# Optimization experiments

Measured on AMD Instinct MI355X. Metric: run time of the kernel, lower is better.

Reference implementation:

```python
import jax, jax.numpy as jnp
import numpy as np

EMBD = 256
HEAD = 4
HD = EMBD // HEAD  # 64
EPS = 1e-5


def setup_inputs() -> dict:
    key = jax.random.key(0)
    ks = jax.random.split(key, 12)
    s = lambda fan_in: 1.0 / np.sqrt(fan_in)
    return {
        "x": jax.random.normal(ks[0], (16, 1024, EMBD), dtype=jnp.float32),
        # attention params (stored as [in, out])
        "qkv_w": jax.random.uniform(ks[1], (EMBD, 3 * EMBD), jnp.float32, -s(EMBD), s(EMBD)),
        "qkv_b": jax.random.uniform(ks[2], (3 * EMBD,), jnp.float32, -s(EMBD), s(EMBD)),
        "out_w": jax.random.uniform(ks[3], (EMBD, EMBD), jnp.float32, -s(EMBD), s(EMBD)),
        "out_b": jax.random.uniform(ks[4], (EMBD,), jnp.float32, -s(EMBD), s(EMBD)),
        # MLP params
        "fc_w": jax.random.uniform(ks[5], (EMBD, 4 * EMBD), jnp.float32, -s(EMBD), s(EMBD)),
        "fc_b": jax.random.uniform(ks[6], (4 * EMBD,), jnp.float32, -s(EMBD), s(EMBD)),
        "proj_w": jax.random.uniform(ks[7], (4 * EMBD, EMBD), jnp.float32, -s(4 * EMBD), s(4 * EMBD)),
        "proj_b": jax.random.uniform(ks[8], (EMBD,), jnp.float32, -s(4 * EMBD), s(4 * EMBD)),
        # LayerNorm params
        "ln1_g": jnp.ones((EMBD,), jnp.float32),
        "ln1_b": jnp.zeros((EMBD,), jnp.float32),
        "ln2_g": jnp.ones((EMBD,), jnp.float32),
        "ln2_b": jnp.zeros((EMBD,), jnp.float32),
    }


def layer_norm(x, g, b):
    mu = jnp.mean(x, axis=-1, keepdims=True)
    var = jnp.mean(jnp.square(x - mu), axis=-1, keepdims=True)
    return (x - mu) * jax.lax.rsqrt(var + EPS) * g + b


def block_forward(x, qkv_w, qkv_b, out_w, out_b, fc_w, fc_b, proj_w, proj_b,
                  ln1_g, ln1_b, ln2_g, ln2_b):
    B, S, E = x.shape
    # --- attention branch ---
    h = layer_norm(x, ln1_g, ln1_b)
    qkv = h @ qkv_w + qkv_b                       # [B,S,3E]
    q, k, v = jnp.split(qkv, 3, axis=-1)
    q = q.reshape(B, S, HEAD, HD).transpose(0, 2, 1, 3)  # [B,H,S,D]
    k = k.reshape(B, S, HEAD, HD).transpose(0, 2, 1, 3)
    v = v.reshape(B, S, HEAD, HD).transpose(0, 2, 1, 3)
    att = jnp.einsum('bhqd,bhkd->bhqk', q, k) / jnp.sqrt(jnp.float32(HD))
    causal = jnp.tril(jnp.ones((S, S), dtype=bool))
    att = jnp.where(causal, att, -jnp.inf)
    att = jax.nn.softmax(att, axis=-1)
    o = jnp.einsum('bhqk,bhkd->bhqd', att, v)     # [B,H,S,D]
    o = o.transpose(0, 2, 1, 3).reshape(B, S, E)
    x = x + o @ out_w + out_b
    # --- MLP branch (dropout inactive at eval) ---
    h = layer_norm(x, ln2_g, ln2_b)
    h = jax.nn.relu(h @ fc_w + fc_b)
    x = x + h @ proj_w + proj_b
    return x


def reference(x, qkv_w, qkv_b, out_w, out_b, fc_w, fc_b, proj_w, proj_b,
              ln1_g, ln1_b, ln2_g, ln2_b):
    return block_forward(x, qkv_w, qkv_b, out_w, out_b, fc_w, fc_b,
                         proj_w, proj_b, ln1_g, ln1_b, ln2_g, ln2_b)
```

## Files before the change

### kernel.cpp

```cpp
#include <hip/hip_runtime.h>
#include <cstdint>


using f32x4 = __attribute__((ext_vector_type(4))) float;
using s16x8 = __attribute__((ext_vector_type(8))) short;
using s16x4 = __attribute__((ext_vector_type(4))) short;

__device__ inline short f2bf(float f) {
    union { float f; unsigned u; } v{f};
    unsigned r = (v.u + 0x7FFFu + ((v.u >> 16) & 1u)) >> 16;
    return (short)r;
}

__device__ inline void gload16(const void* g, void* l) {
    __builtin_amdgcn_global_load_lds(
        (const __attribute__((address_space(1))) void*)g,
        (__attribute__((address_space(3))) void*)l, 16, 0, 0);
}

__global__ __launch_bounds__(256) void wconv_all_kernel(
    const float* __restrict__ qkv_w, const float* __restrict__ out_w,
    const float* __restrict__ fc_w,  const float* __restrict__ proj_w,
    short* __restrict__ wt_qkv, short* __restrict__ wt_out,
    short* __restrict__ wt_fc,  short* __restrict__ wt_proj)
{
    __shared__ short T[64][65];
    int id = blockIdx.x;
    const float* W; short* Wt; int K, N, nt, kt;
    if (id < 48)       { W = qkv_w;  Wt = wt_qkv;  K = 256;  N = 768;  nt = id % 12;        kt = id / 12; }
    else if (id < 64)  { W = out_w;  Wt = wt_out;  K = 256;  N = 256;  nt = (id - 48) & 3;  kt = (id - 48) >> 2; }
    else if (id < 128) { W = fc_w;   Wt = wt_fc;   K = 256;  N = 1024; nt = (id - 64) & 15; kt = (id - 64) >> 4; }
    else               { W = proj_w; Wt = wt_proj; K = 1024; N = 256;  nt = (id - 128) & 3; kt = (id - 128) >> 2; }
    int n0 = nt * 64, k0 = kt * 64;

    int tid = threadIdx.x;
    int r  = tid >> 2;
    int c  = (tid & 3) << 4;

    const float* src = W + (size_t)(k0 + r) * N + n0 + c;
#pragma unroll
    for (int u = 0; u < 4; ++u) {
        float4 v = *reinterpret_cast<const float4*>(src + u * 4);
        T[r][c + u * 4 + 0] = f2bf(v.x);
        T[r][c + u * 4 + 1] = f2bf(v.y);
        T[r][c + u * 4 + 2] = f2bf(v.z);
        T[r][c + u * 4 + 3] = f2bf(v.w);
    }
    __syncthreads();
    s16x8 o0, o1;
#pragma unroll
    for (int j = 0; j < 8; ++j) { o0[j] = T[c + j][r]; o1[j] = T[c + 8 + j][r]; }
    short* dst = Wt + (size_t)(n0 + r) * K + k0 + c;
    *reinterpret_cast<s16x8*>(dst)     = o0;
    *reinterpret_cast<s16x8*>(dst + 8) = o1;
}

__global__ __launch_bounds__(256) void ln_kernel(const float* __restrict__ x,
                                                 const float* __restrict__ gamma,
                                                 const float* __restrict__ beta,
                                                 short* __restrict__ out)
{
    int tid  = threadIdx.x;
    int lane = tid & 63;
    int row  = blockIdx.x * 4 + (tid >> 6);
    const float* xr = x + (size_t)row * 256;
    float4 v = *reinterpret_cast<const float4*>(xr + lane * 4);

    float s = v.x + v.y + v.z + v.w;
#pragma unroll
    for (int o = 32; o >= 1; o >>= 1) s += __shfl_xor(s, o);
    float mu = s * (1.0f / 256.0f);

    float dx = v.x - mu, dy = v.y - mu, dz = v.z - mu, dw = v.w - mu;
    float q = dx * dx + dy * dy + dz * dz + dw * dw;
#pragma unroll
    for (int o = 32; o >= 1; o >>= 1) q += __shfl_xor(q, o);
    float rstd = rsqrtf(q * (1.0f / 256.0f) + 1e-5f);

    float4 gv = *reinterpret_cast<const float4*>(gamma + lane * 4);
    float4 bv = *reinterpret_cast<const float4*>(beta + lane * 4);
    s16x4 ov;
    ov[0] = f2bf(dx * rstd * gv.x + bv.x);
    ov[1] = f2bf(dy * rstd * gv.y + bv.y);
    ov[2] = f2bf(dz * rstd * gv.z + bv.z);
    ov[3] = f2bf(dw * rstd * gv.w + bv.w);
    *reinterpret_cast<s16x4*>(out + (size_t)row * 256 + lane * 4) = ov;
}

template <int RELU, int RES, int OBF16, int BM>
__global__ __launch_bounds__(256) void mgemm_kernel(const short* __restrict__ A,
                                                    const short* __restrict__ Bt,
                                                    const float* __restrict__ bias,
                                                    const float* __restrict__ R,
                                                    void* __restrict__ Cv,
                                                    int N, int K)
{
    constexpr int MI = BM / 32;
    __shared__ short As[BM * 64];
    __shared__ short Bs[128 * 64];

    int tid = threadIdx.x;
    int l   = tid & 63;
    int w   = tid >> 6;
    int lr  = l & 15;
    int lk8 = (l >> 4) << 3;
    int r4  = (l >> 4) << 2;
    int wr  = w >> 1, wc = w & 1;
    int bn  = blockIdx.x * 128, bm = blockIdx.y * BM;

    int scolS = ((l & 7) << 3) ^ ((l >> 3) << 3);
    int srowA = w * (BM / 4) + (l >> 3);
    int srowB = (w << 5) + (l >> 3);
    const short* pa = A  + (size_t)(bm + srowA) * K + scolS;
    const short* pb = Bt + (size_t)(bn + srowB) * K + scolS;
    short* dstA = As + w * (BM / 4) * 64;
    short* dstB = Bs + (w << 11);

    f32x4 acc[MI][4];
#pragma unroll
    for (int mi = 0; mi < MI; ++mi)
#pragma unroll
        for (int ni = 0; ni < 4; ++ni) acc[mi][ni] = (f32x4){0.f, 0.f, 0.f, 0.f};

    int swz = (lr & 7) << 3;

    for (int k0 = 0; k0 < K; k0 += 64) {
        __syncthreads();
#pragma unroll
        for (int i = 0; i < BM / 32; ++i)
            gload16(pa + (size_t)(i * 8) * K + k0, dstA + (i << 9));
#pragma unroll
        for (int i = 0; i < 4; ++i)
            gload16(pb + (size_t)(i * 8) * K + k0, dstB + (i << 9));
        __syncthreads();

#pragma unroll
        for (int ks = 0; ks < 2; ++ks) {
            s16x8 af[MI], bf[4];
#pragma unroll
            for (int mi = 0; mi < MI; ++mi) {
                int row = wr * (BM / 2) + (mi << 4) + lr;
                af[mi] = *reinterpret_cast<const s16x8*>(
                    &As[(row << 6) + (((ks << 5) + lk8) ^ swz)]);
            }
#pragma unroll
            for (int ni = 0; ni < 4; ++ni) {
                int row = (wc << 6) + (ni << 4) + lr;
                bf[ni] = *reinterpret_cast<const s16x8*>(
                    &Bs[(row << 6) + (((ks << 5) + lk8) ^ swz)]);
            }
#pragma unroll
            for (int mi = 0; mi < MI; ++mi)
#pragma unroll
                for (int ni = 0; ni < 4; ++ni)
                    acc[mi][ni] = __builtin_amdgcn_mfma_f32_16x16x32_bf16(
                        af[mi], bf[ni], acc[mi][ni], 0, 0, 0);
        }
    }

    float bv[4];
#pragma unroll
    for (int ni = 0; ni < 4; ++ni)
        bv[ni] = bias[bn + (wc << 6) + (ni << 4) + lr];

#pragma unroll
    for (int mi = 0; mi < MI; ++mi) {
#pragma unroll
        for (int ni = 0; ni < 4; ++ni) {
            int n = bn + (wc << 6) + (ni << 4) + lr;
#pragma unroll
            for (int r = 0; r < 4; ++r) {
                int m = bm + wr * (BM / 2) + (mi << 4) + r4 + r;
                float v = acc[mi][ni][r] + bv[ni];
                if (RELU) v = fmaxf(v, 0.0f);
                if (RES)  v += R[(size_t)m * N + n];
                if (OBF16) ((short*)Cv)[(size_t)m * N + n] = f2bf(v);
                else       ((float*)Cv)[(size_t)m * N + n] = v;
            }
        }
    }
}

__global__ __launch_bounds__(256) void oproj_ln_kernel(const short* __restrict__ A,
                                                       const short* __restrict__ Bt,
                                                       const float* __restrict__ bias,
                                                       const float* __restrict__ R,
                                                       float* __restrict__ x1,
                                                       short* __restrict__ h2,
                                                       const float* __restrict__ g,
                                                       const float* __restrict__ bb)
{
    __shared__ short As[64 * 64];
    __shared__ short Bs[256 * 64];

    int tid = threadIdx.x;
    int l   = tid & 63;
    int w   = tid >> 6;
    int lr  = l & 15;
    int lk8 = (l >> 4) << 3;
    int r4  = (l >> 4) << 2;
    int bm  = blockIdx.x * 64;

    int scolS = ((l & 7) << 3) ^ ((l >> 3) << 3);
    const short* pa = A  + (size_t)(bm + (w << 4) + (l >> 3)) * 256 + scolS;
    const short* pb = Bt + (size_t)((w << 6) + (l >> 3)) * 256 + scolS;
    short* dstA = As + (w << 10);
    short* dstB = Bs + (w << 12);

    f32x4 acc[16];
#pragma unroll
    for (int ni = 0; ni < 16; ++ni) acc[ni] = (f32x4){0.f, 0.f, 0.f, 0.f};

    int swz = (lr & 7) << 3;

    for (int k0 = 0; k0 < 256; k0 += 64) {
        __syncthreads();
#pragma unroll
        for (int i = 0; i < 2; ++i)
            gload16(pa + (size_t)(i * 8) * 256 + k0, dstA + (i << 9));
#pragma unroll
        for (int i = 0; i < 8; ++i)
            gload16(pb + (size_t)(i * 8) * 256 + k0, dstB + (i << 9));
        __syncthreads();

#pragma unroll
        for (int ks = 0; ks < 2; ++ks) {
            int arow = (w << 4) + lr;
            s16x8 af = *reinterpret_cast<const s16x8*>(
                &As[(arow << 6) + (((ks << 5) + lk8) ^ swz)]);
#pragma unroll
            for (int ni = 0; ni < 16; ++ni) {
                int row = (ni << 4) + lr;
                s16x8 bf = *reinterpret_cast<const s16x8*>(
                    &Bs[(row << 6) + (((ks << 5) + lk8) ^ swz)]);
                acc[ni] = __builtin_amdgcn_mfma_f32_16x16x32_bf16(af, bf, acc[ni], 0, 0, 0);
            }
        }
    }

#pragma unroll
    for (int ni = 0; ni < 16; ++ni) {
        int n = (ni << 4) + lr;
        float bvx = bias[n];
#pragma unroll
        for (int r = 0; r < 4; ++r) {
            int m = bm + (w << 4) + r4 + r;
            acc[ni][r] += bvx + R[(size_t)m * 256 + n];
        }
    }
#pragma unroll
    for (int r = 0; r < 4; ++r) {
        float s = 0.0f;
#pragma unroll
        for (int ni = 0; ni < 16; ++ni) s += acc[ni][r];
        s += __shfl_xor(s, 1); s += __shfl_xor(s, 2);
        s += __shfl_xor(s, 4); s += __shfl_xor(s, 8);
        float mu = s * (1.0f / 256.0f);
        float q = 0.0f;
#pragma unroll
        for (int ni = 0; ni < 16; ++ni) {
            float d = acc[ni][r] - mu;
            q += d * d;
        }
        q += __shfl_xor(q, 1); q += __shfl_xor(q, 2);
        q += __shfl_xor(q, 4); q += __shfl_xor(q, 8);
        float rstd = rsqrtf(q * (1.0f / 256.0f) + 1e-5f);

        int m = bm + (w << 4) + r4 + r;
#pragma unroll
        for (int ni = 0; ni < 16; ++ni) {
            int n = (ni << 4) + lr;
            float v = acc[ni][r];
            x1[(size_t)m * 256 + n] = v;
            h2[(size_t)m * 256 + n] = f2bf((v - mu) * rstd * g[n] + bb[n]);
        }
    }
}

__global__ __launch_bounds__(256) void attn_kernel(const short* __restrict__ qkv,
                                                   short* __restrict__ o)
{
    __shared__ short Ks[128 * 64];
    __shared__ short Vt[2 * 64 * 64];
    __shared__ short QP[64 * 128];

    int bid  = blockIdx.x;
    int slot = bid & 7;
    int kk2  = bid >> 3;
    int pair = kk2 & 7;
    int bh   = slot + ((kk2 >> 3) << 3);
    int b = bh >> 2, h = bh & 3;

    int tid  = threadIdx.x;
    const short* base = qkv + (size_t)b * 1024 * 768;

    int l   = tid & 63;
    int w   = tid >> 6;
    int lr  = l & 15;
    int lk8 = (l >> 4) << 3;
    int r4  = (l >> 4) << 2;
    int w16 = w << 4;

    const float SC = 0.125f * 1.44269504088896f;

    for (int sel = 0; sel < 2; ++sel) {
        int qt = sel == 0 ? pair : 15 - pair;

        __syncthreads();
        {
            int qr = tid >> 2;
            int c0 = (tid & 3) << 4;
            int sw = (qr & 7) << 3;
            const short* qg = base + (size_t)(qt * 64 + qr) * 768 + h * 64 + c0;
            s16x8 q0 = *reinterpret_cast<const s16x8*>(qg);
            s16x8 q1 = *reinterpret_cast<const s16x8*>(qg + 8);
            *reinterpret_cast<s16x8*>(&QP[qr * 128 + (c0 ^ sw)])       = q0;
            *reinterpret_cast<s16x8*>(&QP[qr * 128 + ((c0 + 8) ^ sw)]) = q1;
        }
        __syncthreads();

        s16x8 qf[2];
#pragma unroll
        for (int ks = 0; ks < 2; ++ks) {
            int row = w16 + lr;
            qf[ks] = *reinterpret_cast<const s16x8*>(
                &QP[row * 128 + ((lk8 + 32 * ks) ^ ((row & 7) << 3))]);
        }

        float m[4], lsum[4];
        f32x4 oacc[4];
#pragma unroll
        for (int r = 0; r < 4; ++r) { m[r] = -1e30f; lsum[r] = 0.0f; }
#pragma unroll
        for (int jt = 0; jt < 4; ++jt) oacc[jt] = (f32x4){0.f, 0.f, 0.f, 0.f};

        int ntile = qt >> 1;
        for (int kt = 0; kt <= ntile; ++kt) {
            __syncthreads();
            {
                int c0 = (tid & 3) << 4;
#pragma unroll
                for (int i = 0; i < 2; ++i) {
                    int krow = i * 64 + (tid >> 2);
                    const short* kg = base + (size_t)(kt * 128 + krow) * 768 + 256 + h * 64 + c0;
                    s16x8 k0v = *reinterpret_cast<const s16x8*>(kg);
                    s16x8 k1v = *reinterpret_cast<const s16x8*>(kg + 8);
                    int sw = (krow & 7) << 3;
                    *reinterpret_cast<s16x8*>(&Ks[krow * 64 + (c0 ^ sw)])       = k0v;
                    *reinterpret_cast<s16x8*>(&Ks[krow * 64 + ((c0 + 8) ^ sw)]) = k1v;
                    s16x8 v0 = *reinterpret_cast<const s16x8*>(kg + 256);
                    s16x8 v1 = *reinterpret_cast<const s16x8*>(kg + 264);
                    short* vth = Vt + ((krow >> 6) << 12);
                    int kkl = krow & 63;
#pragma unroll
                    for (int e = 0; e < 8; ++e) {
                        int da = c0 + e, db = c0 + 8 + e;
                        vth[da * 64 + (kkl ^ ((da & 7) << 3))] = v0[e];
                        vth[db * 64 + (kkl ^ ((db & 7) << 3))] = v1[e];
                    }
                }
            }
            __syncthreads();

            f32x4 s[8];
#pragma unroll
            for (int jt = 0; jt < 8; ++jt) s[jt] = (f32x4){0.f, 0.f, 0.f, 0.f};
#pragma unroll
            for (int ks = 0; ks < 2; ++ks) {
#pragma unroll
                for (int jt = 0; jt < 8; ++jt) {
                    int row = jt * 16 + lr;
                    s16x8 kf = *reinterpret_cast<const s16x8*>(
                        &Ks[row * 64 + ((lk8 + 32 * ks) ^ ((lr & 7) << 3))]);
                    s[jt] = __builtin_amdgcn_mfma_f32_16x16x32_bf16(qf[ks], kf, s[jt], 0, 0, 0);
                }
            }
#pragma unroll
            for (int jt = 0; jt < 8; ++jt)
#pragma unroll
                for (int r = 0; r < 4; ++r) s[jt][r] *= SC;

            if (kt == ntile) {
#pragma unroll
                for (int jt = 0; jt < 8; ++jt)
#pragma unroll
                    for (int r = 0; r < 4; ++r)
                        if (kt * 128 + jt * 16 + lr > qt * 64 + w16 + r4 + r)
                            s[jt][r] = -1e30f;
            }

#pragma unroll
            for (int r = 0; r < 4; ++r) {
                float rm = s[0][r];
#pragma unroll
                for (int jt = 1; jt < 8; ++jt) rm = fmaxf(rm, s[jt][r]);
                rm = fmaxf(rm, __shfl_xor(rm, 1));
                rm = fmaxf(rm, __shfl_xor(rm, 2));
                rm = fmaxf(rm, __shfl_xor(rm, 4));
                rm = fmaxf(rm, __shfl_xor(rm, 8));
                float mn  = fmaxf(m[r], rm);
                float fct = exp2f(m[r] - mn);
                m[r] = mn;
                float p[8], ps = 0.0f;
#pragma unroll
                for (int jt = 0; jt < 8; ++jt) { p[jt] = exp2f(s[jt][r] - mn); ps += p[jt]; }
                ps += __shfl_xor(ps, 1);
                ps += __shfl_xor(ps, 2);
                ps += __shfl_xor(ps, 4);
                ps += __shfl_xor(ps, 8);
                lsum[r] = lsum[r] * fct + ps;
#pragma unroll
                for (int jt = 0; jt < 4; ++jt) oacc[jt][r] *= fct;
                int row = w16 + r4 + r;
                int sw  = (row & 15) << 3;
                int rb  = row * 128;
#pragma unroll
                for (int jt = 0; jt < 8; ++jt)
                    QP[rb + ((lr + 16 * jt) ^ sw)] = f2bf(p[jt]);
            }

            int prow = w16 + lr;
            int psw  = (prow & 15) << 3;
#pragma unroll
            for (int ks = 0; ks < 4; ++ks) {
                s16x8 pf = *reinterpret_cast<const s16x8*>(
                    &QP[prow * 128 + ((lk8 + 32 * ks) ^ psw)]);
                const short* vth = Vt + ((ks >> 1) << 12);
#pragma unroll
                for (int jt = 0; jt < 4; ++jt) {
                    int vrow = jt * 16 + lr;
                    s16x8 vf = *reinterpret_cast<const s16x8*>(
                        &vth[vrow * 64 + ((((ks & 1) << 5) + lk8) ^ ((lr & 7) << 3))]);
                    oacc[jt] = __builtin_amdgcn_mfma_f32_16x16x32_bf16(pf, vf, oacc[jt], 0, 0, 0);
                }
            }
        }

#pragma unroll
        for (int r = 0; r < 4; ++r) {
            float inv = 1.0f / lsum[r];
            short* orow = o + (size_t)(b * 1024 + qt * 64 + w16 + r4 + r) * 256 + h * 64;
#pragma unroll
            for (int jt = 0; jt < 4; ++jt)
                orow[lr + 16 * jt] = f2bf(oacc[jt][r] * inv);
        }
    }
}

extern "C" void kernel_launch(void* const* d_in, const int* in_sizes, int n_in,
                              void* d_out, int out_size, void* d_ws, size_t ws_size,
                              hipStream_t stream)
{
    const float* x      = (const float*)d_in[0];
    const float* qkv_w  = (const float*)d_in[1];
    const float* qkv_b  = (const float*)d_in[2];
    const float* out_w  = (const float*)d_in[3];
    const float* out_b  = (const float*)d_in[4];
    const float* fc_w   = (const float*)d_in[5];
    const float* fc_b   = (const float*)d_in[6];
    const float* proj_w = (const float*)d_in[7];
    const float* proj_b = (const float*)d_in[8];
    const float* ln1_g  = (const float*)d_in[9];
    const float* ln1_b  = (const float*)d_in[10];
    const float* ln2_g  = (const float*)d_in[11];
    const float* ln2_b  = (const float*)d_in[12];
    float* out = (float*)d_out;

    short* ws = (short*)d_ws;
    short* wt_qkv  = ws;
    short* wt_out  = ws + 196608;
    short* wt_fc   = ws + 262144;
    short* wt_proj = ws + 524288;
    short* bufA    = ws + 786432;
    short* bufB    = ws + 4980736;

    dim3 blk(256);

    wconv_all_kernel<<<dim3(192), blk, 0, stream>>>(
        qkv_w, out_w, fc_w, proj_w, wt_qkv, wt_out, wt_fc, wt_proj);
    ln_kernel<<<dim3(4096), blk, 0, stream>>>(x, ln1_g, ln1_b, bufA);
    mgemm_kernel<0, 0, 1, 128><<<dim3(6, 128), blk, 0, stream>>>(
        bufA, wt_qkv, qkv_b, nullptr, bufB, 768, 256);
    attn_kernel<<<dim3(512), blk, 0, stream>>>(bufB, bufA);
    oproj_ln_kernel<<<dim3(256), blk, 0, stream>>>(
        bufA, wt_out, out_b, x, out, bufA, ln2_g, ln2_b);
    mgemm_kernel<1, 0, 1, 128><<<dim3(8, 128), blk, 0, stream>>>(
        bufA, wt_fc, fc_b, nullptr, bufB, 1024, 256);
    mgemm_kernel<0, 1, 0, 64><<<dim3(2, 256), blk, 0, stream>>>(
        bufB, wt_proj, proj_b, out, out, 256, 1024);
}
```

Before: 138.5 us.

## Keep softmax probabilities in registers via permlane swaps and split attention grid

The attention kernel now computes S transposed (K as the A operand), so each lane holds a column of scores for one query row. It then packs probabilities to bf16 with v_cvt_pk_bf16_f32 and rearranges them with permlane32/16 swaps into the PV MFMA operand layout, removing the LDS round-trip through the QP buffer. The paired query-tile loop per block is replaced by one query tile per block, which doubles the grid to 1024 blocks, and launch bounds request 4 blocks per CU. This adds more blocks with uneven causal work and relies on the cross-lane shuffle layout being correct.

```diff
diff --git a/kernel.cpp b/kernel.cpp
--- a/kernel.cpp
+++ b/kernel.cpp
@@ -10,6 +10,18 @@
     union { float f; unsigned u; } v{f};
     unsigned r = (v.u + 0x7FFFu + ((v.u >> 16) & 1u)) >> 16;
     return (short)r;
+}
+
+__device__ inline int cvt_pk_bf16(float lo, float hi) {
+    int d;
+    asm("v_cvt_pk_bf16_f32 %0, %1, %2" : "=v"(d) : "v"(lo), "v"(hi));
+    return d;
+}
+__device__ inline void swap32(int& a, int& b) {
+    asm("v_permlane32_swap_b32 %0, %1" : "+v"(a), "+v"(b));
+}
+__device__ inline void swap16(int& a, int& b) {
+    asm("v_permlane16_swap_b32 %0, %1" : "+v"(a), "+v"(b));
 }
 
 __device__ inline void gload16(const void* g, void* l) {
@@ -277,173 +289,180 @@
     }
 }
 
-__global__ __launch_bounds__(256) void attn_kernel(const short* __restrict__ qkv,
-                                                   short* __restrict__ o)
+__global__ __launch_bounds__(256, 4) void attn_kernel(const short* __restrict__ qkv,
+                                                      short* __restrict__ o)
 {
+    __shared__ short Qs[64 * 64];
     __shared__ short Ks[128 * 64];
     __shared__ short Vt[2 * 64 * 64];
-    __shared__ short QP[64 * 128];
 
     int bid  = blockIdx.x;
-    int slot = bid & 7;
-    int kk2  = bid >> 3;
-    int pair = kk2 & 7;
-    int bh   = slot + ((kk2 >> 3) << 3);
+    int xcd  = bid & 7;
+    int rest = bid >> 3;
+    int qt   = rest & 15;
+    int bh   = ((rest >> 4) << 3) | xcd;
     int b = bh >> 2, h = bh & 3;
 
-    int tid  = threadIdx.x;
+    int tid = threadIdx.x;
     const short* base = qkv + (size_t)b * 1024 * 768;
 
     int l   = tid & 63;
     int w   = tid >> 6;
     int lr  = l & 15;
-    int lk8 = (l >> 4) << 3;
-    int r4  = (l >> 4) << 2;
+    int g   = l >> 4;
+    int lk8 = g << 3;
     int w16 = w << 4;
+    int qglob = qt * 64 + w16 + lr;
 
     const float SC = 0.125f * 1.44269504088896f;
 
-    for (int sel = 0; sel < 2; ++sel) {
-        int qt = sel == 0 ? pair : 15 - pair;
-
+    {
+        int qr = tid >> 2;
+        int c0 = (tid & 3) << 4;
+        int sw = (qr & 7) << 3;
+        const short* qg = base + (size_t)(qt * 64 + qr) * 768 + h * 64 + c0;
+        s16x8 q0 = *reinterpret_cast<const s16x8*>(qg);
+        s16x8 q1 = *reinterpret_cast<const s16x8*>(qg + 8);
+        *reinterpret_cast<s16x8*>(&Qs[qr * 64 + (c0 ^ sw)])       = q0;
+        *reinterpret_cast<s16x8*>(&Qs[qr * 64 + ((c0 + 8) ^ sw)]) = q1;
+    }
+    __syncthreads();
+
+    s16x8 qf[2];
+#pragma unroll
+    for (int ks = 0; ks < 2; ++ks) {
+        int row = w16 + lr;
+        qf[ks] = *reinterpret_cast<const s16x8*>(
+            &Qs[row * 64 + ((32 * ks + lk8) ^ ((lr & 7) << 3))]);
+    }
+
+    float m = -1e30f, lsum = 0.0f;
+    f32x4 oacc[4];
+#pragma unroll
+    for (int dt = 0; dt < 4; ++dt) oacc[dt] = (f32x4){0.f, 0.f, 0.f, 0.f};
+
+    int ntile = qt >> 1;
+    for (int kt = 0; kt <= ntile; ++kt) {
         __syncthreads();
         {
-            int qr = tid >> 2;
             int c0 = (tid & 3) << 4;
-            int sw = (qr & 7) << 3;
-            const short* qg = base + (size_t)(qt * 64 + qr) * 768 + h * 64 + c0;
-            s16x8 q0 = *reinterpret_cast<const s16x8*>(qg);
-            s16x8 q1 = *reinterpret_cast<const s16x8*>(qg + 8);
-            *reinterpret_cast<s16x8*>(&QP[qr * 128 + (c0 ^ sw)])       = q0;
-            *reinterpret_cast<s16x8*>(&QP[qr * 128 + ((c0 + 8) ^ sw)]) = q1;
+#pragma unroll
+            for (int i = 0; i < 2; ++i) {
+                int krow = i * 64 + (tid >> 2);
+                const short* kg = base + (size_t)(kt * 128 + krow) * 768 + 256 + h * 64 + c0;
+                s16x8 k0v = *reinterpret_cast<const s16x8*>(kg);
+                s16x8 k1v = *reinterpret_cast<const s16x8*>(kg + 8);
+                int sw = (krow & 7) << 3;
+                *reinterpret_cast<s16x8*>(&Ks[krow * 64 + (c0 ^ sw)])       = k0v;
+                *reinterpret_cast<s16x8*>(&Ks[krow * 64 + ((c0 + 8) ^ sw)]) = k1v;
+                s16x8 v0 = *reinterpret_cast<const s16x8*>(kg + 256);
+                s16x8 v1 = *reinterpret_cast<const s16x8*>(kg + 264);
+                short* vth = Vt + ((krow >> 6) << 12);
+                int kkl = krow & 63;
+#pragma unroll
+                for (int e = 0; e < 8; ++e) {
+                    int da = c0 + e, db = c0 + 8 + e;
+                    vth[da * 64 + (kkl ^ ((da & 7) << 3))] = v0[e];
+                    vth[db * 64 + (kkl ^ ((db & 7) << 3))] = v1[e];
+                }
+            }
         }
         __syncthreads();
 
-        s16x8 qf[2];
+        f32x4 s[8];
+#pragma unroll
+        for (int jt = 0; jt < 8; ++jt) s[jt] = (f32x4){0.f, 0.f, 0.f, 0.f};
 #pragma unroll
         for (int ks = 0; ks < 2; ++ks) {
-            int row = w16 + lr;
-            qf[ks] = *reinterpret_cast<const s16x8*>(
-                &QP[row * 128 + ((lk8 + 32 * ks) ^ ((row & 7) << 3))]);
-        }
-
-        float m[4], lsum[4];
-        f32x4 oacc[4];
-#pragma unroll
-        for (int r = 0; r < 4; ++r) { m[r] = -1e30f; lsum[r] = 0.0f; }
-#pragma unroll
-        for (int jt = 0; jt < 4; ++jt) oacc[jt] = (f32x4){0.f, 0.f, 0.f, 0.f};
-
-        int ntile = qt >> 1;
-        for (int kt = 0; kt <= ntile; ++kt) {
-            __syncthreads();
-            {
-                int c0 = (tid & 3) << 4;
-#pragma unroll
-                for (int i = 0; i < 2; ++i) {
-                    int krow = i * 64 + (tid >> 2);
-                    const short* kg = base + (size_t)(kt * 128 + krow) * 768 + 256 + h * 64 + c0;
-                    s16x8 k0v = *reinterpret_cast<const s16x8*>(kg);
-                    s16x8 k1v = *reinterpret_cast<const s16x8*>(kg + 8);
-                    int sw = (krow & 7) << 3;
-                    *reinterpret_cast<s16x8*>(&Ks[krow * 64 + (c0 ^ sw)])       = k0v;
-                    *reinterpret_cast<s16x8*>(&Ks[krow * 64 + ((c0 + 8) ^ sw)]) = k1v;
-                    s16x8 v0 = *reinterpret_cast<const s16x8*>(kg + 256);
-                    s16x8 v1 = *reinterpret_cast<const s16x8*>(kg + 264);
-                    short* vth = Vt + ((krow >> 6) << 12);
-                    int kkl = krow & 63;
-#pragma unroll
-                    for (int e = 0; e < 8; ++e) {
-                        int da = c0 + e, db = c0 + 8 + e;
-                        vth[da * 64 + (kkl ^ ((da & 7) << 3))] = v0[e];
-                        vth[db * 64 + (kkl ^ ((db & 7) << 3))] = v1[e];
-                    }
-                }
-            }
-            __syncthreads();
-
-            f32x4 s[8];
-#pragma unroll
-            for (int jt = 0; jt < 8; ++jt) s[jt] = (f32x4){0.f, 0.f, 0.f, 0.f};
-#pragma unroll
-            for (int ks = 0; ks < 2; ++ks) {
-#pragma unroll
-                for (int jt = 0; jt < 8; ++jt) {
-                    int row = jt * 16 + lr;
-                    s16x8 kf = *reinterpret_cast<const s16x8*>(
-                        &Ks[row * 64 + ((lk8 + 32 * ks) ^ ((lr & 7) << 3))]);
-                    s[jt] = __builtin_amdgcn_mfma_f32_16x16x32_bf16(qf[ks], kf, s[jt], 0, 0, 0);
-                }
-            }
-#pragma unroll
-            for (int jt = 0; jt < 8; ++jt)
-#pragma unroll
-                for (int r = 0; r < 4; ++r) s[jt][r] *= SC;
-
-            if (kt == ntile) {
-#pragma unroll
-                for (int jt = 0; jt < 8; ++jt)
-#pragma unroll
-                    for (int r = 0; r < 4; ++r)
-                        if (kt * 128 + jt * 16 + lr > qt * 64 + w16 + r4 + r)
-                            s[jt][r] = -1e30f;
-            }
-
+#pragma unroll
+            for (int jt = 0; jt < 8; ++jt) {
+                int row = jt * 16 + lr;
+                s16x8 kf = *reinterpret_cast<const s16x8*>(
+                    &Ks[row * 64 + ((32 * ks + lk8) ^ ((lr & 7) << 3))]);
+                s[jt] = __builtin_amdgcn_mfma_f32_16x16x32_bf16(kf, qf[ks], s[jt], 0, 0, 0);
+            }
+        }
+#pragma unroll
+        for (int jt = 0; jt < 8; ++jt)
+#pragma unroll
+            for (int r = 0; r < 4; ++r) s[jt][r] *= SC;
+
+        if (kt == ntile) {
+#pragma unroll
+            for (int jt = 0; jt < 8; ++jt) {
+                int kb = kt * 128 + jt * 16 + 4 * g;
+#pragma unroll
+                for (int r = 0; r < 4; ++r)
+                    if (kb + r > qglob) s[jt][r] = -1e30f;
+            }
+        }
+
+        float rm = fmaxf(fmaxf(s[0][0], s[0][1]), fmaxf(s[0][2], s[0][3]));
+#pragma unroll
+        for (int jt = 1; jt < 8; ++jt) {
+            float t = fmaxf(fmaxf(s[jt][0], s[jt][1]), fmaxf(s[jt][2], s[jt][3]));
+            rm = fmaxf(rm, t);
+        }
+        rm = fmaxf(rm, __shfl_xor(rm, 16));
+        rm = fmaxf(rm, __shfl_xor(rm, 32));
+        float mn  = fmaxf(m, rm);
+        float fct = exp2f(m - mn);
+        m = mn;
+        float ps = 0.0f;
+#pragma unroll
+        for (int jt = 0; jt < 8; ++jt) {
 #pragma unroll
             for (int r = 0; r < 4; ++r) {
-                float rm = s[0][r];
-#pragma unroll
-                for (int jt = 1; jt < 8; ++jt) rm = fmaxf(rm, s[jt][r]);
-                rm = fmaxf(rm, __shfl_xor(rm, 1));
-                rm = fmaxf(rm, __shfl_xor(rm, 2));
-                rm = fmaxf(rm, __shfl_xor(rm, 4));
-                rm = fmaxf(rm, __shfl_xor(rm, 8));
-                float mn  = fmaxf(m[r], rm);
-                float fct = exp2f(m[r] - mn);
-                m[r] = mn;
-                float p[8], ps = 0.0f;
-#pragma unroll
-                for (int jt = 0; jt < 8; ++jt) { p[jt] = exp2f(s[jt][r] - mn); ps += p[jt]; }
-                ps += __shfl_xor(ps, 1);
-                ps += __shfl_xor(ps, 2);
-                ps += __shfl_xor(ps, 4);
-                ps += __shfl_xor(ps, 8);
-                lsum[r] = lsum[r] * fct + ps;
-#pragma unroll
-                for (int jt = 0; jt < 4; ++jt) oacc[jt][r] *= fct;
-                int row = w16 + r4 + r;
-                int sw  = (row & 15) << 3;
-                int rb  = row * 128;
-#pragma unroll
-                for (int jt = 0; jt < 8; ++jt)
-                    QP[rb + ((lr + 16 * jt) ^ sw)] = f2bf(p[jt]);
-            }
-
-            int prow = w16 + lr;
-            int psw  = (prow & 15) << 3;
-#pragma unroll
-            for (int ks = 0; ks < 4; ++ks) {
-                s16x8 pf = *reinterpret_cast<const s16x8*>(
-                    &QP[prow * 128 + ((lk8 + 32 * ks) ^ psw)]);
-                const short* vth = Vt + ((ks >> 1) << 12);
-#pragma unroll
-                for (int jt = 0; jt < 4; ++jt) {
-                    int vrow = jt * 16 + lr;
-                    s16x8 vf = *reinterpret_cast<const s16x8*>(
-                        &vth[vrow * 64 + ((((ks & 1) << 5) + lk8) ^ ((lr & 7) << 3))]);
-                    oacc[jt] = __builtin_amdgcn_mfma_f32_16x16x32_bf16(pf, vf, oacc[jt], 0, 0, 0);
-                }
-            }
+                float p = exp2f(s[jt][r] - mn);
+                s[jt][r] = p;
+                ps += p;
+            }
+        }
+        ps += __shfl_xor(ps, 16);
+        ps += __shfl_xor(ps, 32);
+        lsum = lsum * fct + ps;
+
+        int cpk[8][2];
+#pragma unroll
+        for (int jt = 0; jt < 8; ++jt) {
+            cpk[jt][0] = cvt_pk_bf16(s[jt][0], s[jt][1]);
+            cpk[jt][1] = cvt_pk_bf16(s[jt][2], s[jt][3]);
         }
 
 #pragma unroll
         for (int r = 0; r < 4; ++r) {
-            float inv = 1.0f / lsum[r];
-            short* orow = o + (size_t)(b * 1024 + qt * 64 + w16 + r4 + r) * 256 + h * 64;
-#pragma unroll
-            for (int jt = 0; jt < 4; ++jt)
-                orow[lr + 16 * jt] = f2bf(oacc[jt][r] * inv);
-        }
+            float f4 = __shfl(fct, 4 * g + r);
+#pragma unroll
+            for (int dt = 0; dt < 4; ++dt) oacc[dt][r] *= f4;
+        }
+
+#pragma unroll
+        for (int ks = 0; ks < 4; ++ks) {
+            int a0 = cpk[2 * ks][0],     a1 = cpk[2 * ks][1];
+            int b0 = cpk[2 * ks + 1][0], b1 = cpk[2 * ks + 1][1];
+            swap32(a0, b0); swap32(a1, b1);
+            swap16(a0, b0); swap16(a1, b1);
+            union { int i[4]; s16x8 v; } fr;
+            fr.i[0] = a0; fr.i[1] = a1; fr.i[2] = b0; fr.i[3] = b1;
+            const short* vth = Vt + ((ks >> 1) << 12);
+#pragma unroll
+            for (int dt = 0; dt < 4; ++dt) {
+                int vrow = dt * 16 + lr;
+                s16x8 vf = *reinterpret_cast<const s16x8*>(
+                    &vth[vrow * 64 + ((((ks & 1) << 5) + lk8) ^ ((lr & 7) << 3))]);
+                oacc[dt] = __builtin_amdgcn_mfma_f32_16x16x32_bf16(fr.v, vf, oacc[dt], 0, 0, 0);
+            }
+        }
+    }
+
+#pragma unroll
+    for (int r = 0; r < 4; ++r) {
+        float lv  = __shfl(lsum, 4 * g + r);
+        float inv = 1.0f / lv;
+        short* orow = o + (size_t)(b * 1024 + qt * 64 + w16 + 4 * g + r) * 256 + h * 64;
+#pragma unroll
+        for (int dt = 0; dt < 4; ++dt)
+            orow[dt * 16 + lr] = f2bf(oacc[dt][r] * inv);
     }
 }
 
@@ -481,7 +500,7 @@
     ln_kernel<<<dim3(4096), blk, 0, stream>>>(x, ln1_g, ln1_b, bufA);
     mgemm_kernel<0, 0, 1, 128><<<dim3(6, 128), blk, 0, stream>>>(
         bufA, wt_qkv, qkv_b, nullptr, bufB, 768, 256);
-    attn_kernel<<<dim3(512), blk, 0, stream>>>(bufB, bufA);
+    attn_kernel<<<dim3(1024), blk, 0, stream>>>(bufB, bufA);
     oproj_ln_kernel<<<dim3(256), blk, 0, stream>>>(
         bufA, wt_out, out_b, x, out, bufA, ln2_g, ln2_b);
     mgemm_kernel<1, 0, 1, 128><<<dim3(8, 128), blk, 0, stream>>>(
```

Measured after the change: 137.6 us. No clear change (-0.6%).
